# Kernel tuning notes

Hardware: AMD Instinct MI355X
Metric: run time of the kernel (lower is better)

Reference implementation:

```python
import jax, jax.numpy as jnp
import numpy as np

VOCAB = 4000
HID = 1024


def setup_inputs() -> dict:
    key = jax.random.key(0)
    ks = jax.random.split(key, 8)
    s = 1.0 / np.sqrt(HID)
    inputs = jax.random.randint(ks[0], (64, 256), 0, VOCAB, dtype=jnp.int64)
    h0 = jnp.zeros((1, 64, HID), dtype=jnp.float32)
    # PyTorch GRU params: weight_ih (3H, V), weight_hh (3H, H), biases (3H,)
    W_ih = jax.random.uniform(ks[1], (3 * HID, VOCAB), jnp.float32, -s, s)
    W_hh = jax.random.uniform(ks[2], (3 * HID, HID), jnp.float32, -s, s)
    b_ih = jax.random.uniform(ks[3], (3 * HID,), jnp.float32, -s, s)
    b_hh = jax.random.uniform(ks[4], (3 * HID,), jnp.float32, -s, s)
    W_out = jax.random.uniform(ks[5], (VOCAB, HID), jnp.float32, -s, s)
    b_out = jax.random.uniform(ks[6], (VOCAB,), jnp.float32, -s, s)
    return {"inputs": inputs, "h0": h0, "W_ih": W_ih, "W_hh": W_hh,
            "b_ih": b_ih, "b_hh": b_hh, "W_out": W_out, "b_out": b_out}


def _gru(inputs, h0, W_ih, W_hh, b_ih, b_hh):
    # inputs: (batch, seq) int ids. one_hot(x) @ W_ih.T == W_ih.T[x] exactly,
    # so precompute the input projection for all steps as an embedding lookup.
    x_proj = jnp.take(W_ih.T, inputs.T, axis=0) + b_ih  # (seq, batch, 3H)
    h = h0[0]  # (batch, H)

    def step(h, xp):
        gh = h @ W_hh.T + b_hh                      # (batch, 3H)
        xr, xz, xn = jnp.split(xp, 3, axis=-1)
        hr, hz, hn_ = jnp.split(gh, 3, axis=-1)
        r = jax.nn.sigmoid(xr + hr)
        z = jax.nn.sigmoid(xz + hz)
        n = jnp.tanh(xn + r * hn_)
        h_new = (1.0 - z) * n + z * h
        return h_new, h_new

    hT, outs = jax.lax.scan(step, h, x_proj)  # outs: (seq, batch, H)
    return outs, hT[None]


def reference(inputs, h0, W_ih, W_hh, b_ih, b_hh, W_out, b_out):
    gru_out, hn = _gru(inputs, h0, W_ih, W_hh, b_ih, b_hh)
    logits = gru_out @ W_out.T + b_out            # (seq, batch, V)
    logits = logits.reshape(-1, W_out.shape[0])   # (seq*batch, V)
    return logits, hn
```

## Files before the change

### kernel.cpp

```cpp
#include <hip/hip_runtime.h>
#include <math.h>

#define SEQ 256
#define BATCH 64
#define HID 1024
#define VOCAB 4000
#define H3 (3 * HID)
#define HSLICE (BATCH * HID)

typedef __attribute__((ext_vector_type(8))) short short8;
typedef __attribute__((ext_vector_type(4))) float f32x4;

__device__ inline unsigned short f2bf(float x) {
    unsigned int u = __builtin_bit_cast(unsigned int, x);
    unsigned int r = (u + 0x7fffu + ((u >> 16) & 1u)) >> 16;
    return (unsigned short)r;
}
__device__ inline float bf2f(unsigned short h) {
    unsigned int u = ((unsigned int)h) << 16;
    return __builtin_bit_cast(float, u);
}

__global__ __launch_bounds__(256) void split_kernel(
    const float* __restrict__ W_hh, const float* __restrict__ W_out,
    const float* __restrict__ h0,
    unsigned short* __restrict__ whh_hi, unsigned short* __restrict__ whh_lo,
    unsigned short* __restrict__ wout_hi, unsigned short* __restrict__ wout_lo,
    unsigned short* __restrict__ h0_hi, unsigned short* __restrict__ h0_lo)
{
    const int NW = 3 * HID * HID;
    const int NO = VOCAB * HID;
    const int NH = BATCH * HID;
    const int total = NW + NO + NH;
    for (int i = blockIdx.x * blockDim.x + threadIdx.x; i < total;
         i += gridDim.x * blockDim.x) {
        const float* src; unsigned short *dh, *dl; int off;
        if (i < NW)           { src = W_hh;  dh = whh_hi;  dl = whh_lo;  off = i; }
        else if (i < NW + NO) { src = W_out; dh = wout_hi; dl = wout_lo; off = i - NW; }
        else                  { src = h0;    dh = h0_hi;   dl = h0_lo;   off = i - NW - NO; }
        float x = src[off];
        unsigned short hi = f2bf(x);
        dh[off] = hi;
        dl[off] = f2bf(x - bf2f(hi));
    }
}

__global__ __launch_bounds__(256) void transpose_wih(
    const float* __restrict__ W_ih, float* __restrict__ W_ihT)
{
    __shared__ float tile[32][33];
    const int tx = threadIdx.x & 31;
    const int ty = threadIdx.x >> 5;
    const int r0 = blockIdx.y * 32;
    const int c0 = blockIdx.x * 32;
    #pragma unroll
    for (int k = 0; k < 4; ++k) {
        const int r = ty + k * 8;
        tile[r][tx] = W_ih[(size_t)(r0 + r) * VOCAB + c0 + tx];
    }
    __syncthreads();
    #pragma unroll
    for (int k = 0; k < 4; ++k) {
        const int r = ty + k * 8;
        W_ihT[(size_t)(c0 + r) * H3 + r0 + tx] = tile[tx][r];
    }
}

__global__ void zero_barrier(int* b) {
    b[blockIdx.x * 1024 + threadIdx.x] = 0;
}

__global__ __launch_bounds__(1024) void gru_persist(
    const unsigned short* __restrict__ whh_hi,
    const unsigned short* __restrict__ whh_lo,
    const float* __restrict__ W_ihT,
    const float* __restrict__ b_ih,
    const float* __restrict__ b_hh,
    const float* __restrict__ h0,
    const int* __restrict__ ids,
    unsigned short* ghi,
    unsigned short* glo,
    float* hn_out,
    int* flag)
{
    __shared__ f32x4 red[16][3][64];

    const int tid = threadIdx.x;
    const int w   = tid >> 6;
    const int l   = tid & 63;
    const int bid = blockIdx.x;
    const int grp   = bid & 7;
    const int local = bid >> 3;
    const int jt  = grp * 8 + (local >> 2);
    const int mt  = local & 3;
    const int j0  = jt * 16;
    const int m0  = mt * 16;
    const int col = l & 15, kg = l >> 4;

    const size_t arow   = (size_t)(m0 + col) * HID;
    const size_t brow_r = (size_t)(j0 + col) * HID;
    const size_t brow_z = (size_t)(HID + j0 + col) * HID;
    const size_t brow_n = (size_t)(2 * HID + j0 + col) * HID;
    const int kbase = w * 64 + kg * 8;

    short8 wr_h[2], wr_l[2], wz_h[2], wz_l[2], wn_h[2], wn_l[2];
    #pragma unroll
    for (int c = 0; c < 2; ++c) {
        const int ko = kbase + c * 32;
        wr_h[c] = *(const short8*)(whh_hi + brow_r + ko);
        wr_l[c] = *(const short8*)(whh_lo + brow_r + ko);
        wz_h[c] = *(const short8*)(whh_hi + brow_z + ko);
        wz_l[c] = *(const short8*)(whh_lo + brow_z + ko);
        wn_h[c] = *(const short8*)(whh_hi + brow_n + ko);
        wn_l[c] = *(const short8*)(whh_lo + brow_n + ko);
    }

    const int bi = (tid >> 4) & 15;
    const int cj = tid & 15;
    const int eb = m0 + bi, ej = j0 + cj;
    float hreg = 0.f, xr_n = 0.f, xz_n = 0.f, xn_n = 0.f;
    float bihr = 0.f, bihz = 0.f, bihn = 0.f;
    float bhhr = 0.f, bhhz = 0.f, bhhn = 0.f;
    if (tid < 256) {
        hreg = h0[(size_t)eb * HID + ej];
        bihr = b_ih[ej]; bihz = b_ih[HID + ej]; bihn = b_ih[2 * HID + ej];
        bhhr = b_hh[ej]; bhhz = b_hh[HID + ej]; bhhn = b_hh[2 * HID + ej];
        const int id0 = ids[eb * SEQ];
        const float* xrow = W_ihT + (size_t)id0 * H3;
        xr_n = xrow[ej]; xz_n = xrow[HID + ej]; xn_n = xrow[2 * HID + ej];
    }
    const int lane = ((bi & 15) >> 2) * 16 + cj;
    const int reg  = bi & 3;

    const int myflag = (jt * 4 + mt) * 32;
    const int pollfl = ((4 * w + (l & 3)) * 4 + mt) * 32;

    for (int t = 0; t < SEQ; ++t) {
        if (t > 0) {
            if (l < 4) {
                while (__hip_atomic_load(&flag[pollfl], __ATOMIC_RELAXED,
                                         __HIP_MEMORY_SCOPE_AGENT) < t)
                    __builtin_amdgcn_s_sleep(1);
            }
            asm volatile("" ::: "memory");
        }

        const unsigned short* ah = ghi + (size_t)t * HSLICE;
        const unsigned short* al = glo + (size_t)t * HSLICE;

        f32x4 accr = {0.f, 0.f, 0.f, 0.f};
        f32x4 accz = {0.f, 0.f, 0.f, 0.f};
        f32x4 accn = {0.f, 0.f, 0.f, 0.f};

        #pragma unroll
        for (int c = 0; c < 2; ++c) {
            const int ko = kbase + c * 32;
            short8 a_h = *(const short8*)(ah + arow + ko);
            short8 a_l = *(const short8*)(al + arow + ko);

            accr = __builtin_amdgcn_mfma_f32_16x16x32_bf16(a_h, wr_h[c], accr, 0, 0, 0);
            accr = __builtin_amdgcn_mfma_f32_16x16x32_bf16(a_h, wr_l[c], accr, 0, 0, 0);
            accr = __builtin_amdgcn_mfma_f32_16x16x32_bf16(a_l, wr_h[c], accr, 0, 0, 0);

            accz = __builtin_amdgcn_mfma_f32_16x16x32_bf16(a_h, wz_h[c], accz, 0, 0, 0);
            accz = __builtin_amdgcn_mfma_f32_16x16x32_bf16(a_h, wz_l[c], accz, 0, 0, 0);
            accz = __builtin_amdgcn_mfma_f32_16x16x32_bf16(a_l, wz_h[c], accz, 0, 0, 0);

            accn = __builtin_amdgcn_mfma_f32_16x16x32_bf16(a_h, wn_h[c], accn, 0, 0, 0);
            accn = __builtin_amdgcn_mfma_f32_16x16x32_bf16(a_h, wn_l[c], accn, 0, 0, 0);
            accn = __builtin_amdgcn_mfma_f32_16x16x32_bf16(a_l, wn_h[c], accn, 0, 0, 0);
        }

        red[w][0][l] = accr;
        red[w][1][l] = accz;
        red[w][2][l] = accn;
        __syncthreads();

        if (tid < 256) {
            float sr = 0.f, sz = 0.f, sn = 0.f;
            #pragma unroll
            for (int kk = 0; kk < 16; ++kk) {
                sr += ((const float*)&red[kk][0][lane])[reg];
                sz += ((const float*)&red[kk][1][lane])[reg];
                sn += ((const float*)&red[kk][2][lane])[reg];
            }
            const float xr = xr_n + bihr;
            const float xz = xz_n + bihz;
            const float xn = xn_n + bihn;
            const float hr  = sr + bhhr;
            const float hz  = sz + bhhz;
            const float hn_ = sn + bhhn;
            const float rg = 1.f / (1.f + expf(-(xr + hr)));
            const float zg = 1.f / (1.f + expf(-(xz + hz)));
            const float ng = tanhf(xn + rg * hn_);
            hreg = (1.f - zg) * ng + zg * hreg;

            const unsigned short hh = f2bf(hreg);
            const unsigned short ll = f2bf(hreg - bf2f(hh));
            const unsigned int hh_n = (unsigned int)(unsigned short)
                __shfl_xor((int)hh, 1, 64);
            const unsigned int ll_n = (unsigned int)(unsigned short)
                __shfl_xor((int)ll, 1, 64);
            const size_t ho = (size_t)(t + 1) * HSLICE + (size_t)eb * HID + ej;
            if ((cj & 1) == 0) {
                const unsigned int hp = (unsigned int)hh | (hh_n << 16);
                const unsigned int lp = (unsigned int)ll | (ll_n << 16);
                __hip_atomic_store((unsigned int*)ghi + (ho >> 1), hp,
                                   __ATOMIC_RELAXED, __HIP_MEMORY_SCOPE_AGENT);
                __hip_atomic_store((unsigned int*)glo + (ho >> 1), lp,
                                   __ATOMIC_RELAXED, __HIP_MEMORY_SCOPE_AGENT);
            }

            if (t + 1 < SEQ) {
                const int id2 = ids[eb * SEQ + t + 1];
                const float* xrow = W_ihT + (size_t)id2 * H3;
                xr_n = xrow[ej]; xz_n = xrow[HID + ej]; xn_n = xrow[2 * HID + ej];
            } else {
                hn_out[(size_t)eb * HID + ej] = hreg;
            }
        }

        __syncthreads();
        if (tid == 0) {
            __hip_atomic_store(&flag[myflag], t + 1, __ATOMIC_RELAXED,
                               __HIP_MEMORY_SCOPE_AGENT);
        }
    }
}

__global__ __launch_bounds__(256) void out_gemm_mfma(
    const unsigned short* __restrict__ Ahi_g,
    const unsigned short* __restrict__ Alo_g,
    const unsigned short* __restrict__ Bhi_g,
    const unsigned short* __restrict__ Blo_g,
    const float* __restrict__ bias,
    float* __restrict__ C)
{
    constexpr int BM = 128, BK = 32, LDK = 40;
    __shared__ unsigned short Ah[BM * LDK], Al[BM * LDK];
    __shared__ unsigned short Bh[BM * LDK], Bl[BM * LDK];

    const int tid = threadIdx.x;
    const int l = tid & 63, w = tid >> 6;
    const int wr = w >> 1, wc = w & 1;
    const int col = l & 15, kg = l >> 4;
    const int bid = blockIdx.x;
    const int xcd = bid & 7;
    const int q   = bid >> 3;
    const int yb  = xcd * 4 + (q >> 7);
    const int xb  = q & 127;
    const int m0 = xb * BM;
    const int n0 = yb * BM;

    f32x4 acc[4][4];
    #pragma unroll
    for (int i = 0; i < 4; ++i)
        #pragma unroll
        for (int jt = 0; jt < 4; ++jt)
            acc[i][jt] = (f32x4){0.f, 0.f, 0.f, 0.f};

    for (int kc = 0; kc < HID; kc += BK) {
        __syncthreads();
        #pragma unroll
        for (int i = 0; i < 2; ++i) {
            const int idx = tid + i * 256;
            const int row = idx >> 2, kq = idx & 3;
            const int go = kc + kq * 8;
            *(short8*)(Ah + row * LDK + kq * 8) =
                *(const short8*)(Ahi_g + (size_t)(m0 + row) * HID + go);
            *(short8*)(Al + row * LDK + kq * 8) =
                *(const short8*)(Alo_g + (size_t)(m0 + row) * HID + go);
            const int n = n0 + row;
            short8 vh = {0,0,0,0,0,0,0,0}, vl = {0,0,0,0,0,0,0,0};
            if (n < VOCAB) {
                vh = *(const short8*)(Bhi_g + (size_t)n * HID + go);
                vl = *(const short8*)(Blo_g + (size_t)n * HID + go);
            }
            *(short8*)(Bh + row * LDK + kq * 8) = vh;
            *(short8*)(Bl + row * LDK + kq * 8) = vl;
        }
        __syncthreads();

        short8 af_h[4], af_l[4], bf_h[4], bf_l[4];
        #pragma unroll
        for (int i = 0; i < 4; ++i) {
            const int r = wr * 64 + i * 16 + col;
            af_h[i] = *(const short8*)(Ah + r * LDK + kg * 8);
            af_l[i] = *(const short8*)(Al + r * LDK + kg * 8);
        }
        #pragma unroll
        for (int jt = 0; jt < 4; ++jt) {
            const int r = wc * 64 + jt * 16 + col;
            bf_h[jt] = *(const short8*)(Bh + r * LDK + kg * 8);
            bf_l[jt] = *(const short8*)(Bl + r * LDK + kg * 8);
        }
        #pragma unroll
        for (int i = 0; i < 4; ++i)
            #pragma unroll
            for (int jt = 0; jt < 4; ++jt) {
                acc[i][jt] = __builtin_amdgcn_mfma_f32_16x16x32_bf16(af_h[i], bf_h[jt], acc[i][jt], 0, 0, 0);
                acc[i][jt] = __builtin_amdgcn_mfma_f32_16x16x32_bf16(af_h[i], bf_l[jt], acc[i][jt], 0, 0, 0);
                acc[i][jt] = __builtin_amdgcn_mfma_f32_16x16x32_bf16(af_l[i], bf_h[jt], acc[i][jt], 0, 0, 0);
            }
    }

    #pragma unroll
    for (int i = 0; i < 4; ++i)
        #pragma unroll
        for (int jt = 0; jt < 4; ++jt)
            #pragma unroll
            for (int r = 0; r < 4; ++r) {
                const int m = m0 + wr * 64 + i * 16 + kg * 4 + r;
                const int n = n0 + wc * 64 + jt * 16 + col;
                if (n < VOCAB)
                    C[(size_t)m * VOCAB + n] = acc[i][jt][r] + bias[n];
            }
}

extern "C" void kernel_launch(void* const* d_in, const int* in_sizes, int n_in,
                              void* d_out, int out_size, void* d_ws, size_t ws_size,
                              hipStream_t stream) {
    const int*   inputs = (const int*)d_in[0];
    const float* h0     = (const float*)d_in[1];
    const float* W_ih   = (const float*)d_in[2];
    const float* W_hh   = (const float*)d_in[3];
    const float* b_ih   = (const float*)d_in[4];
    const float* b_hh   = (const float*)d_in[5];
    const float* W_out  = (const float*)d_in[6];
    const float* b_out  = (const float*)d_in[7];
    float* out = (float*)d_out;

    char* p = (char*)d_ws;
    unsigned short* ghi     = (unsigned short*)p; p += (size_t)(SEQ + 1) * HSLICE * 2;
    unsigned short* glo     = (unsigned short*)p; p += (size_t)(SEQ + 1) * HSLICE * 2;
    unsigned short* whh_hi  = (unsigned short*)p; p += (size_t)3 * HID * HID * 2;
    unsigned short* whh_lo  = (unsigned short*)p; p += (size_t)3 * HID * HID * 2;
    unsigned short* wout_hi = (unsigned short*)p; p += (size_t)VOCAB * HID * 2;
    unsigned short* wout_lo = (unsigned short*)p; p += (size_t)VOCAB * HID * 2;
    float* W_ihT            = (float*)p;          p += (size_t)VOCAB * H3 * 4;
    int* bar                = (int*)p;            p += 8192 * 4;

    split_kernel<<<2048, 256, 0, stream>>>(W_hh, W_out, h0,
        whh_hi, whh_lo, wout_hi, wout_lo, ghi , glo );
    transpose_wih<<<dim3(VOCAB / 32, H3 / 32), 256, 0, stream>>>(W_ih, W_ihT);
    zero_barrier<<<8, 1024, 0, stream>>>(bar);

    float* hn_out = out + (size_t)SEQ * BATCH * VOCAB;
    const unsigned short* a_whh_hi = whh_hi;
    const unsigned short* a_whh_lo = whh_lo;
    const float* a_wihT = W_ihT;
    const float* a_bih = b_ih;
    const float* a_bhh = b_hh;
    const float* a_h0 = h0;
    const int* a_ids = inputs;
    unsigned short* a_ghi = ghi;
    unsigned short* a_glo = glo;
    int* a_bar = bar;
    void* kargs[] = { (void*)&a_whh_hi, (void*)&a_whh_lo, (void*)&a_wihT,
                      (void*)&a_bih, (void*)&a_bhh, (void*)&a_h0, (void*)&a_ids,
                      (void*)&a_ghi, (void*)&a_glo, (void*)&hn_out, (void*)&a_bar };
    hipLaunchCooperativeKernel((const void*)gru_persist, dim3(256), dim3(1024),
                               kargs, 0, stream);

    out_gemm_mfma<<<4096, 256, 0, stream>>>(
        ghi + HSLICE, glo + HSLICE, wout_hi, wout_lo, b_out, out);
}
```

Baseline: 1.598 ms.

## Halve GRU block size, use per-wave flags and double-buffered reduction

Shrinks the persistent GRU block from 16 to 8 waves, so each wave covers twice the K range and keeps twice as many W_hh fragments in registers. It replaces the single per-block flag with four per-wave flags that each epilogue wave stores right after writing its slice of h, which removes the trailing __syncthreads. Consumers now poll 32 flags per wave instead of 4. The shared reduction buffer is double-buffered by step parity so the missing second barrier stays safe, at the cost of more register pressure and more polling traffic.

```diff
diff --git a/kernel.cpp b/kernel.cpp
--- a/kernel.cpp
+++ b/kernel.cpp
@@ -70,7 +70,7 @@
     b[blockIdx.x * 1024 + threadIdx.x] = 0;
 }
 
-__global__ __launch_bounds__(1024) void gru_persist(
+__global__ __launch_bounds__(512) void gru_persist(
     const unsigned short* __restrict__ whh_hi,
     const unsigned short* __restrict__ whh_lo,
     const float* __restrict__ W_ihT,
@@ -83,7 +83,7 @@
     float* hn_out,
     int* flag)
 {
-    __shared__ f32x4 red[16][3][64];
+    __shared__ f32x4 red[2][8][3][65];
 
     const int tid = threadIdx.x;
     const int w   = tid >> 6;
@@ -101,11 +101,11 @@
     const size_t brow_r = (size_t)(j0 + col) * HID;
     const size_t brow_z = (size_t)(HID + j0 + col) * HID;
     const size_t brow_n = (size_t)(2 * HID + j0 + col) * HID;
-    const int kbase = w * 64 + kg * 8;
-
-    short8 wr_h[2], wr_l[2], wz_h[2], wz_l[2], wn_h[2], wn_l[2];
-    #pragma unroll
-    for (int c = 0; c < 2; ++c) {
+    const int kbase = w * 128 + kg * 8;
+
+    short8 wr_h[4], wr_l[4], wz_h[4], wz_l[4], wn_h[4], wn_l[4];
+    #pragma unroll
+    for (int c = 0; c < 4; ++c) {
         const int ko = kbase + c * 32;
         wr_h[c] = *(const short8*)(whh_hi + brow_r + ko);
         wr_l[c] = *(const short8*)(whh_lo + brow_r + ko);
@@ -115,9 +115,9 @@
         wn_l[c] = *(const short8*)(whh_lo + brow_n + ko);
     }
 
-    const int bi = (tid >> 4) & 15;
+    const int bi = tid >> 4;
     const int cj = tid & 15;
-    const int eb = m0 + bi, ej = j0 + cj;
+    const int eb = m0 + (bi & 15), ej = j0 + cj;
     float hreg = 0.f, xr_n = 0.f, xz_n = 0.f, xn_n = 0.f;
     float bihr = 0.f, bihz = 0.f, bihn = 0.f;
     float bhhr = 0.f, bhhz = 0.f, bhhn = 0.f;
@@ -132,12 +132,12 @@
     const int lane = ((bi & 15) >> 2) * 16 + cj;
     const int reg  = bi & 3;
 
-    const int myflag = (jt * 4 + mt) * 32;
-    const int pollfl = ((4 * w + (l & 3)) * 4 + mt) * 32;
+    const int myflag = ((jt * 4 + mt) * 4 + w) * 32;
+    const int pollfl = (((w * 8 + (l >> 2)) * 4 + mt) * 4 + (l & 3)) * 32;
 
     for (int t = 0; t < SEQ; ++t) {
         if (t > 0) {
-            if (l < 4) {
+            if (l < 32) {
                 while (__hip_atomic_load(&flag[pollfl], __ATOMIC_RELAXED,
                                          __HIP_MEMORY_SCOPE_AGENT) < t)
                     __builtin_amdgcn_s_sleep(1);
@@ -153,7 +153,7 @@
         f32x4 accn = {0.f, 0.f, 0.f, 0.f};
 
         #pragma unroll
-        for (int c = 0; c < 2; ++c) {
+        for (int c = 0; c < 4; ++c) {
             const int ko = kbase + c * 32;
             short8 a_h = *(const short8*)(ah + arow + ko);
             short8 a_l = *(const short8*)(al + arow + ko);
@@ -171,28 +171,26 @@
             accn = __builtin_amdgcn_mfma_f32_16x16x32_bf16(a_l, wn_h[c], accn, 0, 0, 0);
         }
 
-        red[w][0][l] = accr;
-        red[w][1][l] = accz;
-        red[w][2][l] = accn;
+        const int par = t & 1;
+        red[par][w][0][l] = accr;
+        red[par][w][1][l] = accz;
+        red[par][w][2][l] = accn;
         __syncthreads();
 
         if (tid < 256) {
             float sr = 0.f, sz = 0.f, sn = 0.f;
             #pragma unroll
-            for (int kk = 0; kk < 16; ++kk) {
-                sr += ((const float*)&red[kk][0][lane])[reg];
-                sz += ((const float*)&red[kk][1][lane])[reg];
-                sn += ((const float*)&red[kk][2][lane])[reg];
+            for (int kk = 0; kk < 8; ++kk) {
+                sr += ((const float*)&red[par][kk][0][lane])[reg];
+                sz += ((const float*)&red[par][kk][1][lane])[reg];
+                sn += ((const float*)&red[par][kk][2][lane])[reg];
             }
             const float xr = xr_n + bihr;
             const float xz = xz_n + bihz;
             const float xn = xn_n + bihn;
-            const float hr  = sr + bhhr;
-            const float hz  = sz + bhhz;
-            const float hn_ = sn + bhhn;
-            const float rg = 1.f / (1.f + expf(-(xr + hr)));
-            const float zg = 1.f / (1.f + expf(-(xz + hz)));
-            const float ng = tanhf(xn + rg * hn_);
+            const float rg = 1.f / (1.f + expf(-(xr + sr + bhhr)));
+            const float zg = 1.f / (1.f + expf(-(xz + sz + bhhz)));
+            const float ng = tanhf(xn + rg * (sn + bhhn));
             hreg = (1.f - zg) * ng + zg * hreg;
 
             const unsigned short hh = f2bf(hreg);
@@ -210,7 +208,11 @@
                 __hip_atomic_store((unsigned int*)glo + (ho >> 1), lp,
                                    __ATOMIC_RELAXED, __HIP_MEMORY_SCOPE_AGENT);
             }
-
+            asm volatile("s_waitcnt vmcnt(0)" ::: "memory");
+            if (l == 0) {
+                __hip_atomic_store(&flag[myflag], t + 1, __ATOMIC_RELAXED,
+                                   __HIP_MEMORY_SCOPE_AGENT);
+            }
             if (t + 1 < SEQ) {
                 const int id2 = ids[eb * SEQ + t + 1];
                 const float* xrow = W_ihT + (size_t)id2 * H3;
@@ -218,12 +220,6 @@
             } else {
                 hn_out[(size_t)eb * HID + ej] = hreg;
             }
-        }
-
-        __syncthreads();
-        if (tid == 0) {
-            __hip_atomic_store(&flag[myflag], t + 1, __ATOMIC_RELAXED,
-                               __HIP_MEMORY_SCOPE_AGENT);
         }
     }
 }
@@ -338,12 +334,12 @@
     unsigned short* wout_hi = (unsigned short*)p; p += (size_t)VOCAB * HID * 2;
     unsigned short* wout_lo = (unsigned short*)p; p += (size_t)VOCAB * HID * 2;
     float* W_ihT            = (float*)p;          p += (size_t)VOCAB * H3 * 4;
-    int* bar                = (int*)p;            p += 8192 * 4;
+    int* bar                = (int*)p;            p += 32768 * 4;
 
     split_kernel<<<2048, 256, 0, stream>>>(W_hh, W_out, h0,
         whh_hi, whh_lo, wout_hi, wout_lo, ghi , glo );
     transpose_wih<<<dim3(VOCAB / 32, H3 / 32), 256, 0, stream>>>(W_ih, W_ihT);
-    zero_barrier<<<8, 1024, 0, stream>>>(bar);
+    zero_barrier<<<32, 1024, 0, stream>>>(bar);
 
     float* hn_out = out + (size_t)SEQ * BATCH * VOCAB;
     const unsigned short* a_whh_hi = whh_hi;
@@ -359,7 +355,7 @@
     void* kargs[] = { (void*)&a_whh_hi, (void*)&a_whh_lo, (void*)&a_wihT,
                       (void*)&a_bih, (void*)&a_bhh, (void*)&a_h0, (void*)&a_ids,
                       (void*)&a_ghi, (void*)&a_glo, (void*)&hn_out, (void*)&a_bar };
-    hipLaunchCooperativeKernel((const void*)gru_persist, dim3(256), dim3(1024),
+    hipLaunchCooperativeKernel((const void*)gru_persist, dim3(256), dim3(512),
                                kargs, 0, stream);
 
     out_gemm_mfma<<<4096, 256, 0, stream>>>(
```

Result: slower. 1.770 ms (+10.7%).

## Double-buffer LDS in output GEMM with register prefetch and reorder block mapping

Applied to the files above, without the earlier changes.

The output-projection GEMM now double-buffers its shared-memory tiles. The next K-chunk is loaded from global memory into registers while MFMAs run on the current buffer, and then written into the other buffer. Only one barrier per iteration is needed instead of two. The block-to-tile mapping also changes so that consecutive blocks on an XCD share the same A rows across four N tiles, which should improve L2 reuse. LDS usage doubles and register pressure rises. The GRU gate math is only reformatted.

```diff
diff --git a/kernel.cpp b/kernel.cpp
--- a/kernel.cpp
+++ b/kernel.cpp
@@ -187,12 +187,9 @@
             const float xr = xr_n + bihr;
             const float xz = xz_n + bihz;
             const float xn = xn_n + bihn;
-            const float hr  = sr + bhhr;
-            const float hz  = sz + bhhz;
-            const float hn_ = sn + bhhn;
-            const float rg = 1.f / (1.f + expf(-(xr + hr)));
-            const float zg = 1.f / (1.f + expf(-(xz + hz)));
-            const float ng = tanhf(xn + rg * hn_);
+            const float rg = 1.f / (1.f + expf(-(xr + sr + bhhr)));
+            const float zg = 1.f / (1.f + expf(-(xz + sz + bhhz)));
+            const float ng = tanhf(xn + rg * (sn + bhhn));
             hreg = (1.f - zg) * ng + zg * hreg;
 
             const unsigned short hh = f2bf(hreg);
@@ -237,8 +234,8 @@
     float* __restrict__ C)
 {
     constexpr int BM = 128, BK = 32, LDK = 40;
-    __shared__ unsigned short Ah[BM * LDK], Al[BM * LDK];
-    __shared__ unsigned short Bh[BM * LDK], Bl[BM * LDK];
+    __shared__ unsigned short Ah[2][BM * LDK], Al[2][BM * LDK];
+    __shared__ unsigned short Bh[2][BM * LDK], Bl[2][BM * LDK];
 
     const int tid = threadIdx.x;
     const int l = tid & 63, w = tid >> 6;
@@ -247,11 +244,14 @@
     const int bid = blockIdx.x;
     const int xcd = bid & 7;
     const int q   = bid >> 3;
-    const int yb  = xcd * 4 + (q >> 7);
-    const int xb  = q & 127;
+    const int xb  = q >> 2;
+    const int yb  = xcd * 4 + (q & 3);
     const int m0 = xb * BM;
     const int n0 = yb * BM;
 
+    const int row0 = tid >> 2,        kq0 = tid & 3;
+    const int row1 = (tid + 256) >> 2, kq1 = (tid + 256) & 3;
+
     f32x4 acc[4][4];
     #pragma unroll
     for (int i = 0; i < 4; ++i)
@@ -259,40 +259,57 @@
         for (int jt = 0; jt < 4; ++jt)
             acc[i][jt] = (f32x4){0.f, 0.f, 0.f, 0.f};
 
-    for (int kc = 0; kc < HID; kc += BK) {
+    short8 pAh[2], pAl[2], pBh[2], pBl[2];
+#define PREFETCH(KC)                                                          \
+    {                                                                         \
+        _Pragma("unroll")                                                     \
+        for (int i = 0; i < 2; ++i) {                                         \
+            const int row = i ? row1 : row0;                                  \
+            const int kq  = i ? kq1  : kq0;                                   \
+            const int go  = (KC) + kq * 8;                                    \
+            pAh[i] = *(const short8*)(Ahi_g + (size_t)(m0 + row) * HID + go); \
+            pAl[i] = *(const short8*)(Alo_g + (size_t)(m0 + row) * HID + go); \
+            const int n = n0 + row;                                           \
+            short8 vh = {0,0,0,0,0,0,0,0}, vl = {0,0,0,0,0,0,0,0};            \
+            if (n < VOCAB) {                                                  \
+                vh = *(const short8*)(Bhi_g + (size_t)n * HID + go);          \
+                vl = *(const short8*)(Blo_g + (size_t)n * HID + go);          \
+            }                                                                 \
+            pBh[i] = vh; pBl[i] = vl;                                         \
+        }                                                                     \
+    }
+#define WRITE_LDS(BUF)                                                        \
+    {                                                                         \
+        _Pragma("unroll")                                                     \
+        for (int i = 0; i < 2; ++i) {                                         \
+            const int row = i ? row1 : row0;                                  \
+            const int kq  = i ? kq1  : kq0;                                   \
+            *(short8*)(&Ah[BUF][row * LDK + kq * 8]) = pAh[i];                \
+            *(short8*)(&Al[BUF][row * LDK + kq * 8]) = pAl[i];                \
+            *(short8*)(&Bh[BUF][row * LDK + kq * 8]) = pBh[i];                \
+            *(short8*)(&Bl[BUF][row * LDK + kq * 8]) = pBl[i];                \
+        }                                                                     \
+    }
+
+    PREFETCH(0)
+    WRITE_LDS(0)
+    int cur = 0;
+
+    for (int c = 0; c < HID / BK; ++c) {
         __syncthreads();
-        #pragma unroll
-        for (int i = 0; i < 2; ++i) {
-            const int idx = tid + i * 256;
-            const int row = idx >> 2, kq = idx & 3;
-            const int go = kc + kq * 8;
-            *(short8*)(Ah + row * LDK + kq * 8) =
-                *(const short8*)(Ahi_g + (size_t)(m0 + row) * HID + go);
-            *(short8*)(Al + row * LDK + kq * 8) =
-                *(const short8*)(Alo_g + (size_t)(m0 + row) * HID + go);
-            const int n = n0 + row;
-            short8 vh = {0,0,0,0,0,0,0,0}, vl = {0,0,0,0,0,0,0,0};
-            if (n < VOCAB) {
-                vh = *(const short8*)(Bhi_g + (size_t)n * HID + go);
-                vl = *(const short8*)(Blo_g + (size_t)n * HID + go);
-            }
-            *(short8*)(Bh + row * LDK + kq * 8) = vh;
-            *(short8*)(Bl + row * LDK + kq * 8) = vl;
-        }
-        __syncthreads();
-
+        if (c + 1 < HID / BK) PREFETCH((c + 1) * BK)
         short8 af_h[4], af_l[4], bf_h[4], bf_l[4];
         #pragma unroll
         for (int i = 0; i < 4; ++i) {
             const int r = wr * 64 + i * 16 + col;
-            af_h[i] = *(const short8*)(Ah + r * LDK + kg * 8);
-            af_l[i] = *(const short8*)(Al + r * LDK + kg * 8);
+            af_h[i] = *(const short8*)(&Ah[cur][r * LDK + kg * 8]);
+            af_l[i] = *(const short8*)(&Al[cur][r * LDK + kg * 8]);
         }
         #pragma unroll
         for (int jt = 0; jt < 4; ++jt) {
             const int r = wc * 64 + jt * 16 + col;
-            bf_h[jt] = *(const short8*)(Bh + r * LDK + kg * 8);
-            bf_l[jt] = *(const short8*)(Bl + r * LDK + kg * 8);
+            bf_h[jt] = *(const short8*)(&Bh[cur][r * LDK + kg * 8]);
+            bf_l[jt] = *(const short8*)(&Bl[cur][r * LDK + kg * 8]);
         }
         #pragma unroll
         for (int i = 0; i < 4; ++i)
@@ -302,7 +319,11 @@
                 acc[i][jt] = __builtin_amdgcn_mfma_f32_16x16x32_bf16(af_h[i], bf_l[jt], acc[i][jt], 0, 0, 0);
                 acc[i][jt] = __builtin_amdgcn_mfma_f32_16x16x32_bf16(af_l[i], bf_h[jt], acc[i][jt], 0, 0, 0);
             }
-    }
+        if (c + 1 < HID / BK) WRITE_LDS(cur ^ 1)
+        cur ^= 1;
+    }
+#undef PREFETCH
+#undef WRITE_LDS
 
     #pragma unroll
     for (int i = 0; i < 4; ++i)
```

After: 1.465 ms. -8.3%, faster.
